# Optimization experiments

Measured on AMD Instinct MI355X. Metric: run time of the kernel, lower is better.

## Reference

```python
import jax, jax.numpy as jnp
import numpy as np

COMMITMENT_COST = 0.25


def setup_inputs() -> dict:
    key = jax.random.key(0)
    k1, k2 = jax.random.split(key)
    B, S, D, K = 8, 4096, 256, 1024
    inputs = jax.random.normal(k1, (B, S, D), dtype=jnp.float32)
    attention_mask = jnp.ones((B, S), dtype=jnp.float32)
    codebook = jax.random.normal(k2, (K, D), dtype=jnp.float32)
    return {"inputs": inputs, "attention_mask": attention_mask, "codebook": codebook}


def reference(inputs, attention_mask, codebook):
    # Inference-mode forward of VectorQuantizer (no EMA update / init / revival).
    B, S, D = inputs.shape
    z = inputs.astype(jnp.float32).reshape(-1, D)          # (N, D)
    m = attention_mask.reshape(-1).astype(jnp.float32)     # (N,)

    cb = codebook.astype(jnp.float32)                      # (K, D)
    # squared L2 distances: ||z||^2 - 2 z e^T + ||e||^2
    dist = (jnp.sum(z * z, axis=-1, keepdims=True)
            - 2.0 * jnp.matmul(z, cb.T)
            + jnp.sum(cb * cb, axis=-1)[None, :])          # (N, K)
    idx = jnp.argmin(dist, axis=-1)                        # (N,)
    q = cb[idx]                                            # (N, D) codebook lookup

    n_valid = jnp.sum(m)
    # mse over valid tokens (elementwise mean, matching F.mse_loss on flat_valid)
    diff = z - jax.lax.stop_gradient(q)
    commitment = jnp.sum(m[:, None] * diff * diff) / (n_valid * D)
    vq_loss = COMMITMENT_COST * commitment

    # straight-through estimator; invalid positions zeroed (as in torch scatter)
    q_ste = z + jax.lax.stop_gradient(q - z)
    quantized = (q_ste * m[:, None]).reshape(B, S, D)
    indices = jnp.where(m > 0, idx, 0).reshape(B, S)
    return quantized, vq_loss, indices
```

## Files before the change

### kernel.cpp

```cpp
#include <hip/hip_runtime.h>
#include <cstdint>

typedef short bf16x8 __attribute__((ext_vector_type(8)));
typedef float f32x4  __attribute__((ext_vector_type(4)));

#define TOK    64
#define CH     64
#define NCH    16
#define BUFW   16384
#define MAXC   32

__device__ __forceinline__ unsigned short f2bf(float f) {
  unsigned u = __float_as_uint(f);
  return (unsigned short)((u + 0x7FFFu + ((u >> 16) & 1u)) >> 16);
}
__device__ __forceinline__ uint4 pack8(float4 a, float4 b) {
  uint4 u;
  u.x = (unsigned)f2bf(a.x) | ((unsigned)f2bf(a.y) << 16);
  u.y = (unsigned)f2bf(a.z) | ((unsigned)f2bf(a.w) << 16);
  u.z = (unsigned)f2bf(b.x) | ((unsigned)f2bf(b.y) << 16);
  u.w = (unsigned)f2bf(b.z) | ((unsigned)f2bf(b.w) << 16);
  return u;
}
__device__ __forceinline__ void gload16(const unsigned short* g, unsigned short* l) {
  __builtin_amdgcn_global_load_lds(
      (const __attribute__((address_space(1))) unsigned int*)(const void*)g,
      (__attribute__((address_space(3))) unsigned int*)(void*)l, 16, 0, 0);
}

__global__ __launch_bounds__(256) void vq_prep(const float* __restrict__ cb,
                                               unsigned short* __restrict__ cb_bf,
                                               float* __restrict__ ee,
                                               float* __restrict__ acc2,
                                               int* __restrict__ done_ctr, int K) {
  if (blockIdx.x == 0 && threadIdx.x == 0) {
    acc2[0] = 0.f; acc2[1] = 0.f; *done_ctr = 0;
  }
  int wave = threadIdx.x >> 6, lane = threadIdx.x & 63;
  int k = blockIdx.x * 4 + wave;
  if (k >= K) return;
  float4 v = *reinterpret_cast<const float4*>(cb + (size_t)k * 256 + lane * 4);
  float s = v.x * v.x + v.y * v.y + v.z * v.z + v.w * v.w;
  #pragma unroll
  for (int off = 32; off; off >>= 1) s += __shfl_down(s, off, 64);
  ushort4 b;
  b.x = f2bf(v.x); b.y = f2bf(v.y); b.z = f2bf(v.z); b.w = f2bf(v.w);
  *reinterpret_cast<ushort4*>(cb_bf + (size_t)k * 256 + lane * 4) = b;
  if (lane == 0) ee[k] = s;
}

__global__ __launch_bounds__(256, 2) void vq_main(
    const float* __restrict__ z, const float* __restrict__ cb,
    const unsigned short* __restrict__ cb_bf, const float* __restrict__ ee,
    const float* __restrict__ mask,
    float* __restrict__ out_q, float* __restrict__ out_idx_f,
    float* __restrict__ out_loss, float* __restrict__ acc2,
    int* __restrict__ done_ctr, int nblocks, int K) {
  __shared__ __align__(16) unsigned short sbuf[2 * BUFW];
  __shared__ float ee_lds[1024];
  __shared__ float znorm[TOK];
  __shared__ int   ccnt[TOK];
  __shared__ unsigned short cand[TOK * MAXC];
  __shared__ unsigned short bkbuf[TOK];
  __shared__ float red[8];
  __shared__ bool  last;

  const int t = threadIdx.x;
  const int n0 = blockIdx.x * TOK;
  const int wv = t >> 6, lane = t & 63;
  const int quad = lane >> 4, l15 = lane & 15;
  const int q16 = t & 15;

  ee_lds[t]       = ee[t];
  ee_lds[t + 256] = ee[t + 256];
  ee_lds[t + 512] = ee[t + 512];
  ee_lds[t + 768] = ee[t + 768];
  if (t < TOK) ccnt[t] = 0;

  #pragma unroll
  for (int pass = 0; pass < 4; ++pass) {
    int row = pass * 16 + (t >> 4);
    const float* zr = z + (size_t)(n0 + row) * 256;
    float ssq = 0.f;
    #pragma unroll
    for (int j = 0; j < 2; ++j) {
      float4 a = *reinterpret_cast<const float4*>(zr + q16 * 16 + j * 8);
      float4 b = *reinterpret_cast<const float4*>(zr + q16 * 16 + j * 8 + 4);
      ssq += a.x*a.x + a.y*a.y + a.z*a.z + a.w*a.w
           + b.x*b.x + b.y*b.y + b.z*b.z + b.w*b.w;
      int g = q16 * 2 + j;
      *reinterpret_cast<uint4*>(&sbuf[row * 256 + ((g ^ (row & 7)) * 8)]) = pack8(a, b);
    }
    #pragma unroll
    for (int off = 1; off < 16; off <<= 1) ssq += __shfl_xor(ssq, off, 64);
    if (q16 == 0) znorm[row] = sqrtf(ssq);
  }
  __syncthreads();

  bf16x8 afrag[8];
  float  znreg[4];
  {
    int row = wv * 16 + l15;
    #pragma unroll
    for (int kk = 0; kk < 8; ++kk) {
      int g = (quad + kk * 4) ^ (row & 7);
      afrag[kk] = *reinterpret_cast<const bf16x8*>(&sbuf[row * 256 + g * 8]);
    }
    #pragma unroll
    for (int r = 0; r < 4; ++r)
      znreg[r] = znorm[wv * 16 + quad * 4 + r];
  }
  __syncthreads();

  {
    #pragma unroll
    for (int i = 0; i < 8; ++i) {
      int f = (wv * 8 + i) * 64 + lane;
      int row = f >> 5, slot = f & 31;
      gload16(cb_bf + (size_t)row * 256 + ((slot ^ (row & 7)) * 8),
              &sbuf[(size_t)(wv * 512 + i * 64) * 8]);
    }
  }
  asm volatile("s_waitcnt vmcnt(0)" ::: "memory");
  __syncthreads();

  float amin[4] = {3.4e38f, 3.4e38f, 3.4e38f, 3.4e38f};

  for (int lc = 0; lc < NCH; ++lc) {
    const int kbase = lc * CH;
    unsigned short* cur = &sbuf[(lc & 1) * BUFW];
    unsigned short* nxt = &sbuf[((lc + 1) & 1) * BUFW];
    if (lc < NCH - 1) {
      const unsigned short* base = cb_bf + (size_t)(kbase + CH) * 256;
      #pragma unroll
      for (int i = 0; i < 8; ++i) {
        int f = (wv * 8 + i) * 64 + lane;
        int row = f >> 5, slot = f & 31;
        gload16(base + (size_t)row * 256 + ((slot ^ (row & 7)) * 8),
                nxt + (size_t)(wv * 512 + i * 64) * 8);
      }
    }

    f32x4 acc[4];
    #pragma unroll
    for (int ct = 0; ct < 4; ++ct) acc[ct] = (f32x4){0.f, 0.f, 0.f, 0.f};
    __builtin_amdgcn_s_setprio(1);
    #pragma unroll
    for (int kk = 0; kk < 8; ++kk) {
      int gx = quad + kk * 4;
      bf16x8 b0 = *reinterpret_cast<const bf16x8*>(&cur[(l15)      * 256 + ((gx ^ ( l15       & 7)) * 8)]);
      bf16x8 b1 = *reinterpret_cast<const bf16x8*>(&cur[(16 + l15) * 256 + ((gx ^ ((16 + l15) & 7)) * 8)]);
      bf16x8 b2 = *reinterpret_cast<const bf16x8*>(&cur[(32 + l15) * 256 + ((gx ^ ((32 + l15) & 7)) * 8)]);
      bf16x8 b3 = *reinterpret_cast<const bf16x8*>(&cur[(48 + l15) * 256 + ((gx ^ ((48 + l15) & 7)) * 8)]);
      acc[0] = __builtin_amdgcn_mfma_f32_16x16x32_bf16(afrag[kk], b0, acc[0], 0, 0, 0);
      acc[1] = __builtin_amdgcn_mfma_f32_16x16x32_bf16(afrag[kk], b1, acc[1], 0, 0, 0);
      acc[2] = __builtin_amdgcn_mfma_f32_16x16x32_bf16(afrag[kk], b2, acc[2], 0, 0, 0);
      acc[3] = __builtin_amdgcn_mfma_f32_16x16x32_bf16(afrag[kk], b3, acc[3], 0, 0, 0);
    }
    __builtin_amdgcn_s_setprio(0);

    float e0 = ee_lds[kbase + l15],      e1 = ee_lds[kbase + 16 + l15];
    float e2 = ee_lds[kbase + 32 + l15], e3 = ee_lds[kbase + 48 + l15];
    float en0 = sqrtf(e0), en1 = sqrtf(e1), en2 = sqrtf(e2), en3 = sqrtf(e3);
    #pragma unroll
    for (int r = 0; r < 4; ++r) {
      float d0 = e0 - 2.f * acc[0][r];
      float d1 = e1 - 2.f * acc[1][r];
      float d2 = e2 - 2.f * acc[2][r];
      float d3 = e3 - 2.f * acc[3][r];
      float w = fminf(fminf(d0, d1), fminf(d2, d3));
      #pragma unroll
      for (int off = 1; off < 16; off <<= 1) w = fminf(w, __shfl_xor(w, off, 64));
      float am = fminf(amin[r], w);
      amin[r] = am;
      int tok = wv * 16 + quad * 4 + r;
      float zn = znreg[r];
      if (d0 <= am + 1.5f + 0.002f * zn * en0) {
        int sl = atomicAdd(&ccnt[tok], 1);
        if (sl < MAXC) cand[tok * MAXC + sl] = (unsigned short)(kbase + l15);
      }
      if (d1 <= am + 1.5f + 0.002f * zn * en1) {
        int sl = atomicAdd(&ccnt[tok], 1);
        if (sl < MAXC) cand[tok * MAXC + sl] = (unsigned short)(kbase + 16 + l15);
      }
      if (d2 <= am + 1.5f + 0.002f * zn * en2) {
        int sl = atomicAdd(&ccnt[tok], 1);
        if (sl < MAXC) cand[tok * MAXC + sl] = (unsigned short)(kbase + 32 + l15);
      }
      if (d3 <= am + 1.5f + 0.002f * zn * en3) {
        int sl = atomicAdd(&ccnt[tok], 1);
        if (sl < MAXC) cand[tok * MAXC + sl] = (unsigned short)(kbase + 48 + l15);
      }
    }
    asm volatile("s_waitcnt vmcnt(0)" ::: "memory");
    __syncthreads();
  }

  for (int it = 0; it < 16; ++it) {
    int tok = wv * 16 + it;
    int n = n0 + tok;
    float4 zv = *reinterpret_cast<const float4*>(z + (size_t)n * 256 + lane * 4);
    int cnt = ccnt[tok];
    float bs = 3.4e38f; int bk = 0;
    if (cnt > MAXC) {
      for (int k = 0; k < K; k += 2) {
        float4 ea = *reinterpret_cast<const float4*>(cb + (size_t)k * 256 + lane * 4);
        float4 eb = *reinterpret_cast<const float4*>(cb + (size_t)(k + 1) * 256 + lane * 4);
        float pa = zv.x * ea.x + zv.y * ea.y + zv.z * ea.z + zv.w * ea.w;
        float pb = zv.x * eb.x + zv.y * eb.y + zv.z * eb.z + zv.w * eb.w;
        #pragma unroll
        for (int off = 32; off; off >>= 1) {
          pa += __shfl_xor(pa, off, 64);
          pb += __shfl_xor(pb, off, 64);
        }
        float sa = ee_lds[k] - 2.f * pa;
        float sb = ee_lds[k + 1] - 2.f * pb;
        if (sa < bs) { bs = sa; bk = k; }
        if (sb < bs) { bs = sb; bk = k + 1; }
      }
    } else {
      int c = 0;
      for (; c + 4 <= cnt; c += 4) {
        int k0 = cand[tok * MAXC + c];
        int k1 = cand[tok * MAXC + c + 1];
        int k2 = cand[tok * MAXC + c + 2];
        int k3 = cand[tok * MAXC + c + 3];
        float4 e0 = *reinterpret_cast<const float4*>(cb + (size_t)k0 * 256 + lane * 4);
        float4 e1 = *reinterpret_cast<const float4*>(cb + (size_t)k1 * 256 + lane * 4);
        float4 e2 = *reinterpret_cast<const float4*>(cb + (size_t)k2 * 256 + lane * 4);
        float4 e3 = *reinterpret_cast<const float4*>(cb + (size_t)k3 * 256 + lane * 4);
        float p0 = zv.x * e0.x + zv.y * e0.y + zv.z * e0.z + zv.w * e0.w;
        float p1 = zv.x * e1.x + zv.y * e1.y + zv.z * e1.z + zv.w * e1.w;
        float p2 = zv.x * e2.x + zv.y * e2.y + zv.z * e2.z + zv.w * e2.w;
        float p3 = zv.x * e3.x + zv.y * e3.y + zv.z * e3.z + zv.w * e3.w;
        #pragma unroll
        for (int off = 32; off; off >>= 1) {
          p0 += __shfl_xor(p0, off, 64);
          p1 += __shfl_xor(p1, off, 64);
          p2 += __shfl_xor(p2, off, 64);
          p3 += __shfl_xor(p3, off, 64);
        }
        float s0 = ee_lds[k0] - 2.f * p0;
        float s1 = ee_lds[k1] - 2.f * p1;
        float s2 = ee_lds[k2] - 2.f * p2;
        float s3 = ee_lds[k3] - 2.f * p3;
        if (s0 < bs || (s0 == bs && k0 < bk)) { bs = s0; bk = k0; }
        if (s1 < bs || (s1 == bs && k1 < bk)) { bs = s1; bk = k1; }
        if (s2 < bs || (s2 == bs && k2 < bk)) { bs = s2; bk = k2; }
        if (s3 < bs || (s3 == bs && k3 < bk)) { bs = s3; bk = k3; }
      }
      for (; c < cnt; ++c) {
        int k = cand[tok * MAXC + c];
        float4 ev = *reinterpret_cast<const float4*>(cb + (size_t)k * 256 + lane * 4);
        float dp = zv.x * ev.x + zv.y * ev.y + zv.z * ev.z + zv.w * ev.w;
        #pragma unroll
        for (int off = 32; off; off >>= 1) dp += __shfl_xor(dp, off, 64);
        float s = ee_lds[k] - 2.f * dp;
        if (s < bs || (s == bs && k < bk)) { bs = s; bk = k; }
      }
    }
    bkbuf[tok] = (unsigned short)bk;
  }

  float lsum = 0.f, msum = 0.f;
  for (int it = 0; it < 16; it += 2) {
    int tokA = wv * 16 + it, tokB = tokA + 1;
    int na = n0 + tokA, nb = n0 + tokB;
    int ba = bkbuf[tokA], bb = bkbuf[tokB];
    float4 za = *reinterpret_cast<const float4*>(z + (size_t)na * 256 + lane * 4);
    float4 zb = *reinterpret_cast<const float4*>(z + (size_t)nb * 256 + lane * 4);
    float4 qa = *reinterpret_cast<const float4*>(cb + (size_t)ba * 256 + lane * 4);
    float4 qb = *reinterpret_cast<const float4*>(cb + (size_t)bb * 256 + lane * 4);
    float ma = mask[na], mb = mask[nb];
    float4 oa; oa.x = qa.x * ma; oa.y = qa.y * ma; oa.z = qa.z * ma; oa.w = qa.w * ma;
    float4 ob; ob.x = qb.x * mb; ob.y = qb.y * mb; ob.z = qb.z * mb; ob.w = qb.w * mb;
    *reinterpret_cast<float4*>(out_q + (size_t)na * 256 + lane * 4) = oa;
    *reinterpret_cast<float4*>(out_q + (size_t)nb * 256 + lane * 4) = ob;
    float dxa = za.x - qa.x, dya = za.y - qa.y, dza = za.z - qa.z, dwa = za.w - qa.w;
    float dxb = zb.x - qb.x, dyb = zb.y - qb.y, dzb = zb.z - qb.z, dwb = zb.w - qb.w;
    lsum = fmaf(ma, dxa * dxa + dya * dya + dza * dza + dwa * dwa, lsum);
    lsum = fmaf(mb, dxb * dxb + dyb * dyb + dzb * dzb + dwb * dwb, lsum);
    if (lane == 0) {
      msum += ma + mb;
      out_idx_f[na] = (ma > 0.f) ? (float)ba : 0.f;
      out_idx_f[nb] = (mb > 0.f) ? (float)bb : 0.f;
    }
  }
  #pragma unroll
  for (int off = 32; off; off >>= 1) lsum += __shfl_down(lsum, off, 64);
  if (lane == 0) { red[wv] = lsum; red[4 + wv] = msum; }
  __syncthreads();
  if (t == 0) {
    atomicAdd(&acc2[0], red[0] + red[1] + red[2] + red[3]);
    atomicAdd(&acc2[1], red[4] + red[5] + red[6] + red[7]);
    __threadfence();
    int prev = atomicAdd(done_ctr, 1);
    last = (prev == nblocks - 1);
  }
  __syncthreads();
  if (last && t == 0) {
    float s  = atomicAdd(&acc2[0], 0.0f);
    float nv = atomicAdd(&acc2[1], 0.0f);
    out_loss[0] = (nv > 0.f) ? (0.25f * s / (nv * 256.0f)) : 0.0f;
  }
}

extern "C" void kernel_launch(void* const* d_in, const int* in_sizes, int n_in,
                              void* d_out, int out_size, void* d_ws, size_t ws_size,
                              hipStream_t stream) {
  const float* z    = (const float*)d_in[0];
  const float* mask = (const float*)d_in[1];
  const float* cb   = (const float*)d_in[2];
  const int N = in_sizes[1];
  const int D = 256;
  const int K = in_sizes[2] / D;

  float* wsf  = (float*)d_ws;
  float* acc2 = wsf;
  int*   dctr = (int*)(wsf + 2);
  float* ee   = wsf + 8;
  unsigned short* cb_bf = (unsigned short*)(ee + K);

  float* out_q     = (float*)d_out;
  float* out_loss  = out_q + (size_t)N * D;
  float* out_idx_f = out_loss + 1;

  vq_prep<<<(K + 3) / 4, 256, 0, stream>>>(cb, cb_bf, ee, acc2, dctr, K);
  vq_main<<<N / TOK, 256, 0, stream>>>(z, cb, cb_bf, ee, mask, out_q,
                                       out_idx_f, out_loss, acc2, dctr, N / TOK, K);
}
```

Measured before the change: 175.8 us.

## Halve token tile, split codebook across wave pairs, use padded LDS pitch

```diff
diff --git a/kernel.cpp b/kernel.cpp
--- a/kernel.cpp
+++ b/kernel.cpp
@@ -4,10 +4,9 @@
 typedef short bf16x8 __attribute__((ext_vector_type(8)));
 typedef float f32x4  __attribute__((ext_vector_type(4)));
 
-#define TOK    64
-#define CH     64
-#define NCH    16
-#define BUFW   16384
+#define TOK    32
+#define PITCH  264
+#define CROWS  32
 #define MAXC   32
 
 __device__ __forceinline__ unsigned short f2bf(float f) {
@@ -21,11 +20,6 @@
   u.z = (unsigned)f2bf(b.x) | ((unsigned)f2bf(b.y) << 16);
   u.w = (unsigned)f2bf(b.z) | ((unsigned)f2bf(b.w) << 16);
   return u;
-}
-__device__ __forceinline__ void gload16(const unsigned short* g, unsigned short* l) {
-  __builtin_amdgcn_global_load_lds(
-      (const __attribute__((address_space(1))) unsigned int*)(const void*)g,
-      (__attribute__((address_space(3))) unsigned int*)(void*)l, 16, 0, 0);
 }
 
 __global__ __launch_bounds__(256) void vq_prep(const float* __restrict__ cb,
@@ -49,15 +43,14 @@
   if (lane == 0) ee[k] = s;
 }
 
-__global__ __launch_bounds__(256, 2) void vq_main(
+__global__ __launch_bounds__(256, 4) void vq_main(
     const float* __restrict__ z, const float* __restrict__ cb,
     const unsigned short* __restrict__ cb_bf, const float* __restrict__ ee,
     const float* __restrict__ mask,
     float* __restrict__ out_q, float* __restrict__ out_idx_f,
     float* __restrict__ out_loss, float* __restrict__ acc2,
     int* __restrict__ done_ctr, int nblocks, int K) {
-  __shared__ __align__(16) unsigned short sbuf[2 * BUFW];
-  __shared__ float ee_lds[1024];
+  __shared__ __align__(16) unsigned short buf[64 * PITCH];
   __shared__ float znorm[TOK];
   __shared__ int   ccnt[TOK];
   __shared__ unsigned short cand[TOK * MAXC];
@@ -68,28 +61,24 @@
   const int t = threadIdx.x;
   const int n0 = blockIdx.x * TOK;
   const int wv = t >> 6, lane = t & 63;
+  const int ts = wv & 1, kh = wv >> 1;
   const int quad = lane >> 4, l15 = lane & 15;
   const int q16 = t & 15;
 
-  ee_lds[t]       = ee[t];
-  ee_lds[t + 256] = ee[t + 256];
-  ee_lds[t + 512] = ee[t + 512];
-  ee_lds[t + 768] = ee[t + 768];
   if (t < TOK) ccnt[t] = 0;
 
   #pragma unroll
-  for (int pass = 0; pass < 4; ++pass) {
+  for (int pass = 0; pass < 2; ++pass) {
     int row = pass * 16 + (t >> 4);
     const float* zr = z + (size_t)(n0 + row) * 256;
     float ssq = 0.f;
     #pragma unroll
     for (int j = 0; j < 2; ++j) {
-      float4 a = *reinterpret_cast<const float4*>(zr + q16 * 16 + j * 8);
-      float4 b = *reinterpret_cast<const float4*>(zr + q16 * 16 + j * 8 + 4);
+      float4 a = *reinterpret_cast<const float4*>(zr + q16 * 8 + j * 128);
+      float4 b = *reinterpret_cast<const float4*>(zr + q16 * 8 + j * 128 + 4);
       ssq += a.x*a.x + a.y*a.y + a.z*a.z + a.w*a.w
            + b.x*b.x + b.y*b.y + b.z*b.z + b.w*b.w;
-      int g = q16 * 2 + j;
-      *reinterpret_cast<uint4*>(&sbuf[row * 256 + ((g ^ (row & 7)) * 8)]) = pack8(a, b);
+      *reinterpret_cast<uint4*>(&buf[row * PITCH + q16 * 8 + j * 128]) = pack8(a, b);
     }
     #pragma unroll
     for (int off = 1; off < 16; off <<= 1) ssq += __shfl_xor(ssq, off, 64);
@@ -100,80 +89,62 @@
   bf16x8 afrag[8];
   float  znreg[4];
   {
-    int row = wv * 16 + l15;
+    const unsigned short* za = &buf[(ts * 16 + l15) * PITCH + quad * 8];
+    #pragma unroll
+    for (int kk = 0; kk < 8; ++kk)
+      afrag[kk] = *reinterpret_cast<const bf16x8*>(za + kk * 32);
+    #pragma unroll
+    for (int r = 0; r < 4; ++r)
+      znreg[r] = znorm[ts * 16 + quad * 4 + r];
+  }
+  __syncthreads();
+
+  const int tq = t & 127;
+  const int sq16 = tq & 15, srow = tq >> 4;
+  unsigned short* qbuf = &buf[kh * CROWS * PITCH];
+  const unsigned short* cbh = cb_bf + (size_t)kh * 512 * 256;
+
+  float amin[4] = {3.4e38f, 3.4e38f, 3.4e38f, 3.4e38f};
+
+  for (int lc = 0; lc < 16; ++lc) {
+    const int kbase = kh * 512 + lc * CROWS;
+    #pragma unroll
+    for (int pass = 0; pass < 4; ++pass) {
+      int row = pass * 8 + srow;
+      const unsigned short* src = cbh + (size_t)(lc * CROWS + row) * 256 + sq16 * 8;
+      uint4 v0 = *reinterpret_cast<const uint4*>(src);
+      uint4 v1 = *reinterpret_cast<const uint4*>(src + 128);
+      *reinterpret_cast<uint4*>(&qbuf[row * PITCH + sq16 * 8])       = v0;
+      *reinterpret_cast<uint4*>(&qbuf[row * PITCH + sq16 * 8 + 128]) = v1;
+    }
+    __syncthreads();
+
+    float e0 = ee[kbase + l15], e1 = ee[kbase + 16 + l15];
+
+    f32x4 acc[2];
+    acc[0] = (f32x4){0.f, 0.f, 0.f, 0.f};
+    acc[1] = (f32x4){0.f, 0.f, 0.f, 0.f};
+    __builtin_amdgcn_s_setprio(1);
     #pragma unroll
     for (int kk = 0; kk < 8; ++kk) {
-      int g = (quad + kk * 4) ^ (row & 7);
-      afrag[kk] = *reinterpret_cast<const bf16x8*>(&sbuf[row * 256 + g * 8]);
-    }
-    #pragma unroll
-    for (int r = 0; r < 4; ++r)
-      znreg[r] = znorm[wv * 16 + quad * 4 + r];
-  }
-  __syncthreads();
-
-  {
-    #pragma unroll
-    for (int i = 0; i < 8; ++i) {
-      int f = (wv * 8 + i) * 64 + lane;
-      int row = f >> 5, slot = f & 31;
-      gload16(cb_bf + (size_t)row * 256 + ((slot ^ (row & 7)) * 8),
-              &sbuf[(size_t)(wv * 512 + i * 64) * 8]);
-    }
-  }
-  asm volatile("s_waitcnt vmcnt(0)" ::: "memory");
-  __syncthreads();
-
-  float amin[4] = {3.4e38f, 3.4e38f, 3.4e38f, 3.4e38f};
-
-  for (int lc = 0; lc < NCH; ++lc) {
-    const int kbase = lc * CH;
-    unsigned short* cur = &sbuf[(lc & 1) * BUFW];
-    unsigned short* nxt = &sbuf[((lc + 1) & 1) * BUFW];
-    if (lc < NCH - 1) {
-      const unsigned short* base = cb_bf + (size_t)(kbase + CH) * 256;
-      #pragma unroll
-      for (int i = 0; i < 8; ++i) {
-        int f = (wv * 8 + i) * 64 + lane;
-        int row = f >> 5, slot = f & 31;
-        gload16(base + (size_t)row * 256 + ((slot ^ (row & 7)) * 8),
-                nxt + (size_t)(wv * 512 + i * 64) * 8);
-      }
-    }
-
-    f32x4 acc[4];
-    #pragma unroll
-    for (int ct = 0; ct < 4; ++ct) acc[ct] = (f32x4){0.f, 0.f, 0.f, 0.f};
-    __builtin_amdgcn_s_setprio(1);
-    #pragma unroll
-    for (int kk = 0; kk < 8; ++kk) {
-      int gx = quad + kk * 4;
-      bf16x8 b0 = *reinterpret_cast<const bf16x8*>(&cur[(l15)      * 256 + ((gx ^ ( l15       & 7)) * 8)]);
-      bf16x8 b1 = *reinterpret_cast<const bf16x8*>(&cur[(16 + l15) * 256 + ((gx ^ ((16 + l15) & 7)) * 8)]);
-      bf16x8 b2 = *reinterpret_cast<const bf16x8*>(&cur[(32 + l15) * 256 + ((gx ^ ((32 + l15) & 7)) * 8)]);
-      bf16x8 b3 = *reinterpret_cast<const bf16x8*>(&cur[(48 + l15) * 256 + ((gx ^ ((48 + l15) & 7)) * 8)]);
+      bf16x8 b0 = *reinterpret_cast<const bf16x8*>(&qbuf[(l15)      * PITCH + quad * 8 + kk * 32]);
+      bf16x8 b1 = *reinterpret_cast<const bf16x8*>(&qbuf[(16 + l15) * PITCH + quad * 8 + kk * 32]);
       acc[0] = __builtin_amdgcn_mfma_f32_16x16x32_bf16(afrag[kk], b0, acc[0], 0, 0, 0);
       acc[1] = __builtin_amdgcn_mfma_f32_16x16x32_bf16(afrag[kk], b1, acc[1], 0, 0, 0);
-      acc[2] = __builtin_amdgcn_mfma_f32_16x16x32_bf16(afrag[kk], b2, acc[2], 0, 0, 0);
-      acc[3] = __builtin_amdgcn_mfma_f32_16x16x32_bf16(afrag[kk], b3, acc[3], 0, 0, 0);
     }
     __builtin_amdgcn_s_setprio(0);
 
-    float e0 = ee_lds[kbase + l15],      e1 = ee_lds[kbase + 16 + l15];
-    float e2 = ee_lds[kbase + 32 + l15], e3 = ee_lds[kbase + 48 + l15];
-    float en0 = sqrtf(e0), en1 = sqrtf(e1), en2 = sqrtf(e2), en3 = sqrtf(e3);
+    float en0 = sqrtf(e0), en1 = sqrtf(e1);
     #pragma unroll
     for (int r = 0; r < 4; ++r) {
       float d0 = e0 - 2.f * acc[0][r];
       float d1 = e1 - 2.f * acc[1][r];
-      float d2 = e2 - 2.f * acc[2][r];
-      float d3 = e3 - 2.f * acc[3][r];
-      float w = fminf(fminf(d0, d1), fminf(d2, d3));
+      float w = fminf(d0, d1);
       #pragma unroll
       for (int off = 1; off < 16; off <<= 1) w = fminf(w, __shfl_xor(w, off, 64));
       float am = fminf(amin[r], w);
       amin[r] = am;
-      int tok = wv * 16 + quad * 4 + r;
+      int tok = ts * 16 + quad * 4 + r;
       float zn = znreg[r];
       if (d0 <= am + 1.5f + 0.002f * zn * en0) {
         int sl = atomicAdd(&ccnt[tok], 1);
@@ -183,21 +154,12 @@
         int sl = atomicAdd(&ccnt[tok], 1);
         if (sl < MAXC) cand[tok * MAXC + sl] = (unsigned short)(kbase + 16 + l15);
       }
-      if (d2 <= am + 1.5f + 0.002f * zn * en2) {
-        int sl = atomicAdd(&ccnt[tok], 1);
-        if (sl < MAXC) cand[tok * MAXC + sl] = (unsigned short)(kbase + 32 + l15);
-      }
-      if (d3 <= am + 1.5f + 0.002f * zn * en3) {
-        int sl = atomicAdd(&ccnt[tok], 1);
-        if (sl < MAXC) cand[tok * MAXC + sl] = (unsigned short)(kbase + 48 + l15);
-      }
-    }
-    asm volatile("s_waitcnt vmcnt(0)" ::: "memory");
+    }
     __syncthreads();
   }
 
-  for (int it = 0; it < 16; ++it) {
-    int tok = wv * 16 + it;
+  for (int it = 0; it < 8; ++it) {
+    int tok = wv * 8 + it;
     int n = n0 + tok;
     float4 zv = *reinterpret_cast<const float4*>(z + (size_t)n * 256 + lane * 4);
     int cnt = ccnt[tok];
@@ -213,8 +175,8 @@
           pa += __shfl_xor(pa, off, 64);
           pb += __shfl_xor(pb, off, 64);
         }
-        float sa = ee_lds[k] - 2.f * pa;
-        float sb = ee_lds[k + 1] - 2.f * pb;
+        float sa = ee[k] - 2.f * pa;
+        float sb = ee[k + 1] - 2.f * pb;
         if (sa < bs) { bs = sa; bk = k; }
         if (sb < bs) { bs = sb; bk = k + 1; }
       }
@@ -240,10 +202,10 @@
           p2 += __shfl_xor(p2, off, 64);
           p3 += __shfl_xor(p3, off, 64);
         }
-        float s0 = ee_lds[k0] - 2.f * p0;
-        float s1 = ee_lds[k1] - 2.f * p1;
-        float s2 = ee_lds[k2] - 2.f * p2;
-        float s3 = ee_lds[k3] - 2.f * p3;
+        float s0 = ee[k0] - 2.f * p0;
+        float s1 = ee[k1] - 2.f * p1;
+        float s2 = ee[k2] - 2.f * p2;
+        float s3 = ee[k3] - 2.f * p3;
         if (s0 < bs || (s0 == bs && k0 < bk)) { bs = s0; bk = k0; }
         if (s1 < bs || (s1 == bs && k1 < bk)) { bs = s1; bk = k1; }
         if (s2 < bs || (s2 == bs && k2 < bk)) { bs = s2; bk = k2; }
@@ -255,7 +217,7 @@
         float dp = zv.x * ev.x + zv.y * ev.y + zv.z * ev.z + zv.w * ev.w;
         #pragma unroll
         for (int off = 32; off; off >>= 1) dp += __shfl_xor(dp, off, 64);
-        float s = ee_lds[k] - 2.f * dp;
+        float s = ee[k] - 2.f * dp;
         if (s < bs || (s == bs && k < bk)) { bs = s; bk = k; }
       }
     }
@@ -263,8 +225,8 @@
   }
 
   float lsum = 0.f, msum = 0.f;
-  for (int it = 0; it < 16; it += 2) {
-    int tokA = wv * 16 + it, tokB = tokA + 1;
+  for (int it = 0; it < 8; it += 2) {
+    int tokA = wv * 8 + it, tokB = tokA + 1;
     int na = n0 + tokA, nb = n0 + tokB;
     int ba = bkbuf[tokA], bb = bkbuf[tokB];
     float4 za = *reinterpret_cast<const float4*>(z + (size_t)na * 256 + lane * 4);
```

New measurement: 315.5 us. 79.5% more time.

## Track per-lane top-4 packed distance keys and defer candidate filtering to the end

Applied to the files above, without the earlier changes.

```diff
diff --git a/kernel.cpp b/kernel.cpp
--- a/kernel.cpp
+++ b/kernel.cpp
@@ -9,6 +9,9 @@
 #define NCH    16
 #define BUFW   16384
 #define MAXC   32
+
+static __device__ __forceinline__ unsigned umn(unsigned a, unsigned b) { return a < b ? a : b; }
+static __device__ __forceinline__ unsigned umx(unsigned a, unsigned b) { return a > b ? a : b; }
 
 __device__ __forceinline__ unsigned short f2bf(float f) {
   unsigned u = __float_as_uint(f);
@@ -71,11 +74,13 @@
   const int quad = lane >> 4, l15 = lane & 15;
   const int q16 = t & 15;
 
-  ee_lds[t]       = ee[t];
-  ee_lds[t + 256] = ee[t + 256];
-  ee_lds[t + 512] = ee[t + 512];
-  ee_lds[t + 768] = ee[t + 768];
+  float ea = ee[t], eb = ee[t + 256], ec = ee[t + 512], ed = ee[t + 768];
+  ee_lds[t] = ea; ee_lds[t + 256] = eb; ee_lds[t + 512] = ec; ee_lds[t + 768] = ed;
   if (t < TOK) ccnt[t] = 0;
+  float em = fmaxf(fmaxf(ea, eb), fmaxf(ec, ed));
+  #pragma unroll
+  for (int off = 32; off; off >>= 1) em = fmaxf(em, __shfl_xor(em, off, 64));
+  if (lane == 0) red[wv] = em;
 
   #pragma unroll
   for (int pass = 0; pass < 4; ++pass) {
@@ -97,6 +102,8 @@
   }
   __syncthreads();
 
+  const float enmax = sqrtf(fmaxf(fmaxf(red[0], red[1]), fmaxf(red[2], red[3])));
+
   bf16x8 afrag[8];
   float  znreg[4];
   {
@@ -124,7 +131,11 @@
   asm volatile("s_waitcnt vmcnt(0)" ::: "memory");
   __syncthreads();
 
-  float amin[4] = {3.4e38f, 3.4e38f, 3.4e38f, 3.4e38f};
+  unsigned pk[4][4];
+  #pragma unroll
+  for (int r = 0; r < 4; ++r)
+    #pragma unroll
+    for (int j = 0; j < 4; ++j) pk[r][j] = 0x7F7FFFFFu;
 
   for (int lc = 0; lc < NCH; ++lc) {
     const int kbase = lc * CH;
@@ -161,53 +172,67 @@
 
     float e0 = ee_lds[kbase + l15],      e1 = ee_lds[kbase + 16 + l15];
     float e2 = ee_lds[kbase + 32 + l15], e3 = ee_lds[kbase + 48 + l15];
-    float en0 = sqrtf(e0), en1 = sqrtf(e1), en2 = sqrtf(e2), en3 = sqrtf(e3);
     #pragma unroll
     for (int r = 0; r < 4; ++r) {
       float d0 = e0 - 2.f * acc[0][r];
       float d1 = e1 - 2.f * acc[1][r];
       float d2 = e2 - 2.f * acc[2][r];
       float d3 = e3 - 2.f * acc[3][r];
-      float w = fminf(fminf(d0, d1), fminf(d2, d3));
+      unsigned pu, tt;
       #pragma unroll
-      for (int off = 1; off < 16; off <<= 1) w = fminf(w, __shfl_xor(w, off, 64));
-      float am = fminf(amin[r], w);
-      amin[r] = am;
-      int tok = wv * 16 + quad * 4 + r;
-      float zn = znreg[r];
-      if (d0 <= am + 1.5f + 0.002f * zn * en0) {
-        int sl = atomicAdd(&ccnt[tok], 1);
-        if (sl < MAXC) cand[tok * MAXC + sl] = (unsigned short)(kbase + l15);
-      }
-      if (d1 <= am + 1.5f + 0.002f * zn * en1) {
-        int sl = atomicAdd(&ccnt[tok], 1);
-        if (sl < MAXC) cand[tok * MAXC + sl] = (unsigned short)(kbase + 16 + l15);
-      }
-      if (d2 <= am + 1.5f + 0.002f * zn * en2) {
-        int sl = atomicAdd(&ccnt[tok], 1);
-        if (sl < MAXC) cand[tok * MAXC + sl] = (unsigned short)(kbase + 32 + l15);
-      }
-      if (d3 <= am + 1.5f + 0.002f * zn * en3) {
-        int sl = atomicAdd(&ccnt[tok], 1);
-        if (sl < MAXC) cand[tok * MAXC + sl] = (unsigned short)(kbase + 48 + l15);
+      for (int ct = 0; ct < 4; ++ct) {
+        float dd = (ct == 0) ? d0 : (ct == 1) ? d1 : (ct == 2) ? d2 : d3;
+        pu = (__float_as_uint(fmaxf(dd, 0.f)) & 0xFFFFFC00u)
+           | (unsigned)(kbase + ct * 16 + l15);
+        tt = umn(pk[r][0], pu); pu = umx(pk[r][0], pu); pk[r][0] = tt;
+        tt = umn(pk[r][1], pu); pu = umx(pk[r][1], pu); pk[r][1] = tt;
+        tt = umn(pk[r][2], pu); pu = umx(pk[r][2], pu); pk[r][2] = tt;
+        pk[r][3] = umn(pk[r][3], pu);
       }
     }
     asm volatile("s_waitcnt vmcnt(0)" ::: "memory");
     __syncthreads();
+  }
+
+  #pragma unroll
+  for (int r = 0; r < 4; ++r) {
+    unsigned w = pk[r][0];
+    #pragma unroll
+    for (int off = 1; off < 16; off <<= 1)
+      w = umn(w, (unsigned)__shfl_xor((int)w, off, 64));
+    float mhat = __uint_as_float(w & 0xFFFFFC00u);
+    float thr = mhat + 1.75f + 0.002f * znreg[r] * enmax;
+    bool f0 = __uint_as_float(pk[r][0] & 0xFFFFFC00u) <= thr;
+    bool f1 = __uint_as_float(pk[r][1] & 0xFFFFFC00u) <= thr;
+    bool f2 = __uint_as_float(pk[r][2] & 0xFFFFFC00u) <= thr;
+    bool f3 = __uint_as_float(pk[r][3] & 0xFFFFFC00u) <= thr;
+    unsigned long long gm = 0xFFFFull << (quad << 4);
+    int n = __popcll(__ballot(f0) & gm) + __popcll(__ballot(f1) & gm)
+          + __popcll(__ballot(f2) & gm) + __popcll(__ballot(f3) & gm);
+    int tok = wv * 16 + quad * 4 + r;
+    if (n == 1) {
+      if (l15 == 0) bkbuf[tok] = (unsigned short)(w & 1023u);
+    } else {
+      if (f0) { int sl = atomicAdd(&ccnt[tok], 1); if (sl < MAXC) cand[tok * MAXC + sl] = (unsigned short)(pk[r][0] & 1023u); }
+      if (f1) { int sl = atomicAdd(&ccnt[tok], 1); if (sl < MAXC) cand[tok * MAXC + sl] = (unsigned short)(pk[r][1] & 1023u); }
+      if (f2) { int sl = atomicAdd(&ccnt[tok], 1); if (sl < MAXC) cand[tok * MAXC + sl] = (unsigned short)(pk[r][2] & 1023u); }
+      if (f3) { atomicAdd(&ccnt[tok], 1000); }
+    }
   }
 
   for (int it = 0; it < 16; ++it) {
     int tok = wv * 16 + it;
     int n = n0 + tok;
+    int cnt = ccnt[tok];
+    if (cnt == 0) continue;
     float4 zv = *reinterpret_cast<const float4*>(z + (size_t)n * 256 + lane * 4);
-    int cnt = ccnt[tok];
     float bs = 3.4e38f; int bk = 0;
     if (cnt > MAXC) {
       for (int k = 0; k < K; k += 2) {
-        float4 ea = *reinterpret_cast<const float4*>(cb + (size_t)k * 256 + lane * 4);
-        float4 eb = *reinterpret_cast<const float4*>(cb + (size_t)(k + 1) * 256 + lane * 4);
-        float pa = zv.x * ea.x + zv.y * ea.y + zv.z * ea.z + zv.w * ea.w;
-        float pb = zv.x * eb.x + zv.y * eb.y + zv.z * eb.z + zv.w * eb.w;
+        float4 ca = *reinterpret_cast<const float4*>(cb + (size_t)k * 256 + lane * 4);
+        float4 cbv = *reinterpret_cast<const float4*>(cb + (size_t)(k + 1) * 256 + lane * 4);
+        float pa = zv.x * ca.x + zv.y * ca.y + zv.z * ca.z + zv.w * ca.w;
+        float pb = zv.x * cbv.x + zv.y * cbv.y + zv.z * cbv.z + zv.w * cbv.w;
         #pragma unroll
         for (int off = 32; off; off >>= 1) {
           pa += __shfl_xor(pa, off, 64);
@@ -219,6 +244,7 @@
         if (sb < bs) { bs = sb; bk = k + 1; }
       }
     } else {
+      bk = 1 << 29;
       int c = 0;
       for (; c + 4 <= cnt; c += 4) {
         int k0 = cand[tok * MAXC + c];
```

New measurement: 351.9 us. +100.2%, slower.
